# Performance work log

Hardware: AMD Instinct MI355X
Metric: run time of the kernel (lower is better)

Reference implementation:

```python
import jax, jax.numpy as jnp
import numpy as np

K = 20
EPS = 1e-5
NEG_SLOPE = 0.2


def knn_idx(feat, k):
    # feat: (B, N, C). Pairwise neg squared distance, top-k nearest (self included).
    inner = jnp.einsum('bnc,bmc->bnm', feat, feat)          # (B,N,N)
    sq = jnp.sum(feat * feat, axis=-1)                      # (B,N)
    pd = 2.0 * inner - sq[:, :, None] - sq[:, None, :]      # -||xi-xj||^2
    return jax.lax.top_k(pd, k)[1]                          # (B,N,k)


def edge_conv(feat, W, g, b, m, v, k):
    # feat: (B,N,C); W: (O, 2C); BN params over O channels (eval-mode BN).
    idx = knn_idx(feat, k)                                  # (B,N,k)
    nbr = jnp.take_along_axis(feat[:, None, :, :], idx[..., None], axis=2)  # (B,N,k,C)
    ctr = jnp.broadcast_to(feat[:, :, None, :], nbr.shape)
    edge = jnp.concatenate([nbr - ctr, ctr], axis=-1)       # (B,N,k,2C)
    h = jnp.einsum('bnkc,oc->bnko', edge, W)                # 1x1 conv
    h = (h - m) * (g / jnp.sqrt(v + EPS)) + b               # BatchNorm2d (eval)
    h = jnp.where(h >= 0, h, NEG_SLOPE * h)                 # LeakyReLU(0.2)
    return jnp.max(h, axis=2)                               # max over k -> (B,N,O)


def setup_inputs() -> dict:
    key = jax.random.key(0)
    ks = jax.random.split(key, 21)
    B, N, C = 4, 4096, 3
    d = {'x': jax.random.normal(ks[0], (B, N, C), dtype=jnp.float32)}
    dims = [(64, 2 * 3), (64, 2 * 64), (128, 2 * 64), (256, 2 * 128)]
    for i, (o, c) in enumerate(dims, start=1):
        j = 1 + (i - 1) * 5
        d[f'W{i}'] = jax.random.normal(ks[j], (o, c), dtype=jnp.float32) * (1.0 / np.sqrt(c))
        d[f'g{i}'] = jax.random.uniform(ks[j + 1], (o,), minval=0.5, maxval=1.5, dtype=jnp.float32)
        d[f'b{i}'] = jax.random.normal(ks[j + 2], (o,), dtype=jnp.float32) * 0.1
        d[f'm{i}'] = jax.random.normal(ks[j + 3], (o,), dtype=jnp.float32) * 0.1
        d[f'v{i}'] = jax.random.uniform(ks[j + 4], (o,), minval=0.5, maxval=1.5, dtype=jnp.float32)
    return d


def reference(x, W1, g1, b1, m1, v1, W2, g2, b2, m2, v2,
              W3, g3, b3, m3, v3, W4, g4, b4, m4, v4):
    x1 = edge_conv(x, W1, g1, b1, m1, v1, K)    # (B,N,64)
    x2 = edge_conv(x1, W2, g2, b2, m2, v2, K)   # (B,N,64)
    x3 = edge_conv(x2, W3, g3, b3, m3, v3, K)   # (B,N,128)
    x4 = edge_conv(x3, W4, g4, b4, m4, v4, K)   # (B,N,256)
    return x4
```

## Files before the change

### kernel.cpp

```cpp
#include <hip/hip_runtime.h>

#define NTOT 4096
#define NBATCH 4
#define KNN 20
#define JSPLIT 8
#define KMRG 24
#define CSLOTM 512

constexpr float NEG_INF = -3.0e38f;

typedef __attribute__((ext_vector_type(8))) short bf16x8;
typedef __attribute__((ext_vector_type(4))) float f32x4;

__device__ __forceinline__ unsigned pk(float f, int j) {
  unsigned u = __float_as_uint(f);
  u = (u & 0x80000000u) ? ~u : (u | 0x80000000u);
  return (u & 0xFFFFF000u) | (unsigned)j;
}

__device__ __forceinline__ void pins8(unsigned u, unsigned (&tv)[8]) {
  if (u > tv[0]) {
    tv[0] = u;
#pragma unroll
    for (int x = 1; x < 8; x++) {
      unsigned mn = min(tv[0], tv[x]);
      unsigned mx = max(tv[0], tv[x]);
      tv[0] = mn;
      tv[x] = mx;
    }
  }
}

__device__ __forceinline__ void sbf16(float x, ushort& h16, ushort& l16) {
  unsigned u = __float_as_uint(x);
  unsigned h = (u + 0x7FFFu + ((u >> 16) & 1u)) >> 16;
  float hf = __uint_as_float(h << 16);
  float r = x - hf;
  unsigned v = __float_as_uint(r);
  unsigned l = (v + 0x7FFFu + ((v >> 16) & 1u)) >> 16;
  h16 = (ushort)h;
  l16 = (ushort)l;
}

__device__ __forceinline__ void gll16(const void* g, void* l) {
  __builtin_amdgcn_global_load_lds(
      (const __attribute__((address_space(1))) unsigned int*)g,
      (__attribute__((address_space(3))) unsigned int*)l, 16, 0, 0);
}

__global__ void prep_w(const float* __restrict__ W, const float* __restrict__ gg,
                       const float* __restrict__ bb, const float* __restrict__ mm,
                       const float* __restrict__ vv, float* __restrict__ Wc,
                       float* __restrict__ bias, int O, int C) {
  int t = blockIdx.x * 256 + threadIdx.x;
  if (t >= 2 * O * C) return;
  int o2 = t / C, c = t - o2 * C;
  int o = (o2 < O) ? o2 : o2 - O;
  float s = gg[o] * rsqrtf(vv[o] + 1e-5f);
  float w = (o2 < O) ? W[o * 2 * C + c] * s
                     : (W[o * 2 * C + C + c] - W[o * 2 * C + c]) * s;
  Wc[o2 * C + c] = w;
  if (o2 >= O && c == 0) bias[o] = bb[o] - mm[o] * s;
}

__global__ void cvt3_k(const float* __restrict__ f, ushort* __restrict__ hi,
                       ushort* __restrict__ lo) {
  int p = blockIdx.x * 256 + threadIdx.x;
  int pt = p >> 5, dim = p & 31;
  float x = (dim < 3) ? f[pt * 3 + dim] : 0.f;
  ushort h16, l16;
  sbf16(x, h16, l16);
  hi[p] = h16;
  lo[p] = l16;
}

__global__ void sqh3_k(const float* __restrict__ f, float* __restrict__ sqh) {
  int p = blockIdx.x * 256 + threadIdx.x;
  float a = f[(size_t)p * 3 + 0];
  float b2 = f[(size_t)p * 3 + 1];
  float c = f[(size_t)p * 3 + 2];
  sqh[p] = 0.5f * (a * a + b2 * b2 + c * c);
}

template <int C>
__global__ __launch_bounds__(1024, 8) void knn_m(const ushort* __restrict__ Xhi,
                                                 const ushort* __restrict__ Xlo,
                                                 const float* __restrict__ sqh,
                                                 unsigned* __restrict__ cval) {
  constexpr int NK = C / 32;
  constexpr int NJT = NTOT / (128 * JSPLIT);
  constexpr int NSQ = 2 * NJT;
  __shared__ __align__(16) char smem[69632];
  float* sqB = (float*)(smem + 65536);

  int tid = threadIdx.x;
  int raw = blockIdx.x;
  int b = raw & 3;
  int jsp = (raw >> 3) & 3;
  int it = (((raw >> 5) & 15) << 1) | ((raw >> 2) & 1);
  int i0 = it * 128;
  int jpbase = jsp * 1024;
  const ushort* xh = Xhi + (size_t)b * NTOT * C;
  const ushort* xl = Xlo + (size_t)b * NTOT * C;

  int l = tid & 63, wid = tid >> 6;
  int wi = wid & 7, wj = wid >> 3;
  int n = l & 15, quad = l >> 4;
  int xr16 = (n & 7) << 4;

  int t0 = l & 1, t1 = (l >> 1) & 1, t2 = (l >> 2) & 1, t3 = (l >> 3) & 1,
      t4 = (l >> 4) & 1, t5 = (l >> 5) & 1;
  int Rl = (t2 ^ t4) | (t3 << 1) | (t4 << 2) | (t5 << 3);
  int ql = (t0 ^ t2 ^ t4) | ((t1 ^ t3) << 1);

  if (tid < 256) {
    float4 s4 = *(const float4*)&sqh[b * NTOT + jpbase + tid * 4];
    *(float4*)&sqB[tid * 4] = s4;
  }
  __syncthreads();

  unsigned tv[8];
#pragma unroll
  for (int x = 0; x < 8; x++) tv[x] = 0u;

  auto issue = [&](int sn, int kcn, char* buf) {
    int band = wid & 7;
    int R = Rl + band * 16;
    char* ld = buf + band * 1024;
    if (wid < 8) {
      size_t gA = (size_t)(i0 + R) * C + kcn + ql * 8;
      gll16(xh + gA, ld);
      gll16(xl + gA, ld + 8192);
    } else {
      int j0n = jpbase + sn * 128;
      size_t gB = (size_t)(j0n + R) * C + kcn + ql * 8;
      gll16(xh + gB, ld + 16384);
      gll16(xl + gB, ld + 24576);
    }
  };

  issue(0, 0, smem);

  int g = 0;
  for (int s = 0; s < NSQ; s++) {
    int j0 = jpbase + s * 128;

    f32x4 acc[4];
#pragma unroll
    for (int tj = 0; tj < 4; tj++) acc[tj] = (f32x4)(0.f);

    for (int kc = 0; kc < NK; kc++) {
      __builtin_amdgcn_s_barrier();
      int nsn = (kc + 1 < NK) ? s : ((s + 1 == NSQ) ? 0 : s + 1);
      int nkc = (kc + 1 < NK) ? (kc + 1) * 32 : 0;
      issue(nsn, nkc, smem + ((g + 1) & 1) * 32768);
      asm volatile("s_waitcnt vmcnt(2)" ::: "memory");
      __builtin_amdgcn_s_barrier();
      const char* bc = smem + (g & 1) * 32768;

      int arow = wi * 16 + n;
      int aoff = (arow * 64 + quad * 16) ^ xr16;
      bf16x8 ah = *(const bf16x8*)(bc + aoff);
      bf16x8 al_ = *(const bf16x8*)(bc + 8192 + aoff);
#pragma unroll
      for (int tj = 0; tj < 4; tj++) {
        int brow = wj * 64 + tj * 16 + n;
        int boff = (brow * 64 + quad * 16) ^ xr16;
        bf16x8 bh = *(const bf16x8*)(bc + 16384 + boff);
        bf16x8 bl = *(const bf16x8*)(bc + 24576 + boff);
        acc[tj] = __builtin_amdgcn_mfma_f32_16x16x32_bf16(bh, ah, acc[tj], 0, 0, 0);
        acc[tj] = __builtin_amdgcn_mfma_f32_16x16x32_bf16(bh, al_, acc[tj], 0, 0, 0);
        acc[tj] = __builtin_amdgcn_mfma_f32_16x16x32_bf16(bl, ah, acc[tj], 0, 0, 0);
      }
      g++;
    }

    float4 sq4[4];
#pragma unroll
    for (int tj = 0; tj < 4; tj++)
      sq4[tj] = *(const float4*)&sqB[s * 128 + wj * 64 + tj * 16 + quad * 4];
#pragma unroll
    for (int tj = 0; tj < 4; tj++) {
      float v0 = acc[tj][0] - sq4[tj].x;
      float v1 = acc[tj][1] - sq4[tj].y;
      float v2 = acc[tj][2] - sq4[tj].z;
      float v3 = acc[tj][3] - sq4[tj].w;
      float m4 = fmaxf(fmaxf(v0, v1), fmaxf(v2, v3));
      if (pk(m4, 0xFFF) > tv[0]) {
        int jb = j0 + wj * 64 + tj * 16 + quad * 4;
        pins8(pk(v0, jb + 0), tv);
        pins8(pk(v1, jb + 1), tv);
        pins8(pk(v2, jb + 2), tv);
        pins8(pk(v3, jb + 3), tv);
      }
    }

    if (s == NJT - 1 || s == NSQ - 1) {
      int js = jsp * 2 + ((s == NSQ - 1) ? 1 : 0);
      int p = b * NTOT + i0 + wi * 16 + n;
      unsigned* dst = cval + (size_t)p * CSLOTM + js * 64 + wj * 32 + quad * 8;
      uint4 o0, o1;
      o0.x = tv[0]; o0.y = tv[1]; o0.z = tv[2]; o0.w = tv[3];
      o1.x = tv[4]; o1.y = tv[5]; o1.z = tv[6]; o1.w = tv[7];
      *(uint4*)&dst[0] = o0;
      *(uint4*)&dst[4] = o1;
#pragma unroll
      for (int x = 0; x < 8; x++) tv[x] = 0u;
    }
  }
}

template <int C, int NC>
__global__ __launch_bounds__(256) void kref_w(const float* __restrict__ feat,
                                              const unsigned* __restrict__ cval,
                                              int* __restrict__ outidx) {
  int tid = threadIdx.x;
  int lane = tid & 63;
  int pbase = blockIdx.x * 8 + (tid >> 6) * 2;

  unsigned c[2][8];
  int bq[2], iq[2];
#pragma unroll
  for (int pt = 0; pt < 2; pt++) {
    int p = pbase + pt;
    bq[pt] = p >> 12;
    iq[pt] = p & (NTOT - 1);
    uint4 aa = *(const uint4*)&cval[(size_t)p * NC + lane * 8];
    uint4 bb2 = *(const uint4*)&cval[(size_t)p * NC + lane * 8 + 4];
    c[pt][0] = aa.x; c[pt][1] = aa.y; c[pt][2] = aa.z; c[pt][3] = aa.w;
    c[pt][4] = bb2.x; c[pt][5] = bb2.y; c[pt][6] = bb2.z; c[pt][7] = bb2.w;
  }

#define CE(a, bq2)                          \
  {                                         \
    unsigned mx = max(c[pt][a], c[pt][bq2]); \
    unsigned mn = min(c[pt][a], c[pt][bq2]); \
    c[pt][a] = mx;                          \
    c[pt][bq2] = mn;                        \
  }
#pragma unroll
  for (int pt = 0; pt < 2; pt++) {
    CE(0, 1) CE(2, 3) CE(4, 5) CE(6, 7)
    CE(0, 2) CE(1, 3) CE(4, 6) CE(5, 7)
    CE(1, 2) CE(5, 6) CE(0, 4) CE(3, 7)
    CE(1, 5) CE(2, 6)
    CE(1, 4) CE(3, 6)
    CE(2, 4) CE(3, 5)
    CE(3, 4)
  }
#undef CE

  int myj[2] = {-1, -1};
#pragma unroll
  for (int t = 0; t < KMRG; t++) {
#pragma unroll
    for (int pt = 0; pt < 2; pt++) {
      unsigned m = c[pt][0];
#pragma unroll
      for (int s = 1; s < 64; s <<= 1)
        m = max(m, (unsigned)__shfl_xor((int)m, s));
      if (lane == t) myj[pt] = (int)(m & 0xFFFu);
      bool mine = (c[pt][0] == m);
      c[pt][0] = mine ? c[pt][1] : c[pt][0];
      c[pt][1] = mine ? c[pt][2] : c[pt][1];
      c[pt][2] = mine ? c[pt][3] : c[pt][2];
      c[pt][3] = mine ? c[pt][4] : c[pt][3];
      c[pt][4] = mine ? c[pt][5] : c[pt][4];
      c[pt][5] = mine ? c[pt][6] : c[pt][5];
      c[pt][6] = mine ? c[pt][7] : c[pt][6];
      c[pt][7] = mine ? 0u : c[pt][7];
    }
  }

  float myval[2] = {NEG_INF, NEG_INF};
  if constexpr (C == 3) {
#pragma unroll
    for (int pt = 0; pt < 2; pt++) {
      const float* fb = feat + (size_t)bq[pt] * NTOT * 3;
      if (lane < KMRG) {
        float x0 = fb[(size_t)iq[pt] * 3 + 0];
        float x1 = fb[(size_t)iq[pt] * 3 + 1];
        float x2 = fb[(size_t)iq[pt] * 3 + 2];
        float y0 = fb[(size_t)myj[pt] * 3 + 0];
        float y1 = fb[(size_t)myj[pt] * 3 + 1];
        float y2 = fb[(size_t)myj[pt] * 3 + 2];
        float d0 = x0 - y0, d1 = x1 - y1, d2 = x2 - y2;
        myval[pt] = -(d0 * d0 + d1 * d1 + d2 * d2);
      }
    }
  } else {
    constexpr int SL = C / 8;
    int m8 = lane & 7;
    float4 xs[2][SL / 4];
#pragma unroll
    for (int pt = 0; pt < 2; pt++)
#pragma unroll
      for (int q4 = 0; q4 < SL / 4; q4++)
        xs[pt][q4] = *(const float4*)&feat[((size_t)bq[pt] * NTOT + iq[pt]) * C +
                                           m8 * SL + q4 * 4];
#pragma unroll
    for (int ps = 0; ps < KMRG / 8; ps++) {
      int src = ps * 8 + (lane >> 3);
#pragma unroll
      for (int pt = 0; pt < 2; pt++) {
        int j = __shfl(myj[pt], src);
        float d = 0.f;
#pragma unroll
        for (int q4 = 0; q4 < SL / 4; q4++) {
          float4 yv = *(const float4*)&feat[((size_t)bq[pt] * NTOT + j) * C +
                                            m8 * SL + q4 * 4];
          float dx = xs[pt][q4].x - yv.x;
          float dy = xs[pt][q4].y - yv.y;
          float dz = xs[pt][q4].z - yv.z;
          float dw = xs[pt][q4].w - yv.w;
          d += dx * dx + dy * dy + dz * dz + dw * dw;
        }
#pragma unroll
        for (int s = 1; s < 8; s <<= 1) d += __shfl_xor(d, s);
        float sd = __shfl(d, (lane & 7) << 3);
        bool upd = ((lane >> 3) == ps);
        myval[pt] = upd ? -sd : myval[pt];
      }
    }
  }

#pragma unroll
  for (int k = 2; k <= 64; k <<= 1) {
#pragma unroll
    for (int j2 = k >> 1; j2 > 0; j2 >>= 1) {
#pragma unroll
      for (int pt = 0; pt < 2; pt++) {
        float ov = __shfl_xor(myval[pt], j2);
        int oj = __shfl_xor(myj[pt], j2);
        bool ogt = (ov > myval[pt]) || (ov == myval[pt] && oj < myj[pt]);
        bool lower = ((lane & j2) == 0);
        bool desc = ((lane & k) == 0);
        bool take = (desc == (lower == ogt));
        myval[pt] = take ? ov : myval[pt];
        myj[pt] = take ? oj : myj[pt];
      }
    }
  }

#pragma unroll
  for (int pt = 0; pt < 2; pt++)
    if (lane < KNN) outidx[(size_t)(pbase + pt) * KNN + lane] = myj[pt];
}

__global__ __launch_bounds__(256) void gemm128(const float* __restrict__ A,
                                               const float* __restrict__ Wc,
                                               const float* __restrict__ bias,
                                               float* __restrict__ Y, int K, int N2,
                                               int O) {
  constexpr int P = 140;
  __shared__ float As[16 * P];
  __shared__ float Bs[16 * P];
  int tid = threadIdx.x;
  int n0 = blockIdx.x * 128;
  int m0 = blockIdx.y * 128;
  int tx = tid & 15, ty = tid >> 4;
  int aoff = (ty * 8) + (((ty * 8) >> 5) << 2);
  int boff = (tx * 8) + (((tx * 8) >> 5) << 2);
  float acc[8][8];
#pragma unroll
  for (int ii = 0; ii < 8; ii++)
#pragma unroll
    for (int jj = 0; jj < 8; jj++) acc[ii][jj] = 0.f;

  for (int kc = 0; kc < K; kc += 16) {
    __syncthreads();
#pragma unroll
    for (int l = 0; l < 2; l++) {
      int e = tid + 256 * l;
      int rr = e >> 2, c4 = e & 3;
      int sc = rr + ((rr >> 5) << 2);
      float4 va = *(const float4*)&A[(size_t)(m0 + rr) * K + kc + c4 * 4];
      As[(c4 * 4 + 0) * P + sc] = va.x;
      As[(c4 * 4 + 1) * P + sc] = va.y;
      As[(c4 * 4 + 2) * P + sc] = va.z;
      As[(c4 * 4 + 3) * P + sc] = va.w;
      float4 vb = *(const float4*)&Wc[(size_t)(n0 + rr) * K + kc + c4 * 4];
      Bs[(c4 * 4 + 0) * P + sc] = vb.x;
      Bs[(c4 * 4 + 1) * P + sc] = vb.y;
      Bs[(c4 * 4 + 2) * P + sc] = vb.z;
      Bs[(c4 * 4 + 3) * P + sc] = vb.w;
    }
    __syncthreads();
#pragma unroll 8
    for (int k = 0; k < 16; k++) {
      float4 a0 = *(const float4*)&As[k * P + aoff];
      float4 a1 = *(const float4*)&As[k * P + aoff + 4];
      float4 b0 = *(const float4*)&Bs[k * P + boff];
      float4 b1 = *(const float4*)&Bs[k * P + boff + 4];
      float av[8] = {a0.x, a0.y, a0.z, a0.w, a1.x, a1.y, a1.z, a1.w};
      float bv[8] = {b0.x, b0.y, b0.z, b0.w, b1.x, b1.y, b1.z, b1.w};
#pragma unroll
      for (int ii = 0; ii < 8; ii++)
#pragma unroll
        for (int jj = 0; jj < 8; jj++)
          acc[ii][jj] = fmaf(av[ii], bv[jj], acc[ii][jj]);
    }
  }

  int col0 = n0 + tx * 8;
  float bv[8];
#pragma unroll
  for (int jj = 0; jj < 8; jj++) {
    int col = col0 + jj;
    bv[jj] = (col >= O) ? bias[col - O] : 0.f;
  }
#pragma unroll
  for (int ii = 0; ii < 8; ii++) {
    int row = m0 + ty * 8 + ii;
    float4 o0, o1;
    o0.x = acc[ii][0] + bv[0];
    o0.y = acc[ii][1] + bv[1];
    o0.z = acc[ii][2] + bv[2];
    o0.w = acc[ii][3] + bv[3];
    o1.x = acc[ii][4] + bv[4];
    o1.y = acc[ii][5] + bv[5];
    o1.z = acc[ii][6] + bv[6];
    o1.w = acc[ii][7] + bv[7];
    *(float4*)&Y[(size_t)row * N2 + col0] = o0;
    *(float4*)&Y[(size_t)row * N2 + col0 + 4] = o1;
  }
}

__global__ __launch_bounds__(256) void gemm_k(const float* __restrict__ A,
                                              const float* __restrict__ Wc,
                                              const float* __restrict__ bias,
                                              float* __restrict__ Y, int K, int N2,
                                              int O) {
  __shared__ float As[8 * 68];
  __shared__ float Bs[8 * 68];
  int tid = threadIdx.x;
  int n0 = blockIdx.x * 64;
  int m0 = blockIdx.y * 64;
  int tx = tid & 15, ty = tid >> 4;
  float acc[4][4] = {};
  for (int k0 = 0; k0 < K; k0 += 8) {
    __syncthreads();
    {
      int e = tid, mm = e >> 3, kk = e & 7;
      As[kk * 68 + mm] = (k0 + kk < K) ? A[(size_t)(m0 + mm) * K + k0 + kk] : 0.f;
      int nn = mm;
      Bs[kk * 68 + nn] = (k0 + kk < K) ? Wc[(size_t)(n0 + nn) * K + k0 + kk] : 0.f;
      e = tid + 256;
      mm = e >> 3;
      kk = e & 7;
      As[kk * 68 + mm] = (k0 + kk < K) ? A[(size_t)(m0 + mm) * K + k0 + kk] : 0.f;
      nn = mm;
      Bs[kk * 68 + nn] = (k0 + kk < K) ? Wc[(size_t)(n0 + nn) * K + k0 + kk] : 0.f;
    }
    __syncthreads();
#pragma unroll
    for (int kk = 0; kk < 8; kk++) {
      float4 av = *(float4*)&As[kk * 68 + ty * 4];
      float4 bv = *(float4*)&Bs[kk * 68 + tx * 4];
      float a[4] = {av.x, av.y, av.z, av.w};
      float bb2[4] = {bv.x, bv.y, bv.z, bv.w};
#pragma unroll
      for (int ii = 0; ii < 4; ii++)
#pragma unroll
        for (int jj = 0; jj < 4; jj++) acc[ii][jj] += a[ii] * bb2[jj];
    }
  }
  int col = n0 + tx * 4;
  bool isV = (col >= O);
  float b0 = 0.f, b1 = 0.f, b2 = 0.f, b3 = 0.f;
  if (isV) {
    b0 = bias[col + 0 - O];
    b1 = bias[col + 1 - O];
    b2 = bias[col + 2 - O];
    b3 = bias[col + 3 - O];
  }
#pragma unroll
  for (int ii = 0; ii < 4; ii++) {
    int row = m0 + ty * 4 + ii;
    float4 o4;
    o4.x = acc[ii][0] + b0;
    o4.y = acc[ii][1] + b1;
    o4.z = acc[ii][2] + b2;
    o4.w = acc[ii][3] + b3;
    *(float4*)&Y[(size_t)row * N2 + col] = o4;
  }
}

template <int O, int CN>
__global__ __launch_bounds__(256) void gmax_v(const float* __restrict__ Y,
                                              const int* __restrict__ idx,
                                              float* __restrict__ out,
                                              ushort* __restrict__ nxh,
                                              ushort* __restrict__ nxl,
                                              float* __restrict__ nsq) {
  constexpr int T = O / 4;
  constexpr int G = 256 / T;
  int tid = threadIdx.x;
  int p = blockIdx.x * G + tid / T;
  int o4 = (tid % T) * 4;
  int b = p >> 12;
  constexpr int N2 = 2 * O;
  const int* ip = idx + (size_t)p * KNN;
  float4 m = make_float4(NEG_INF, NEG_INF, NEG_INF, NEG_INF);
#pragma unroll
  for (int k = 0; k < KNN; k++) {
    int j = ip[k];
    float4 v = *(const float4*)&Y[((size_t)(b * NTOT + j)) * N2 + o4];
    m.x = fmaxf(m.x, v.x);
    m.y = fmaxf(m.y, v.y);
    m.z = fmaxf(m.z, v.z);
    m.w = fmaxf(m.w, v.w);
  }
  float4 c = *(const float4*)&Y[(size_t)p * N2 + O + o4];
  float4 o;
  o.x = c.x + m.x;
  o.y = c.y + m.y;
  o.z = c.z + m.z;
  o.w = c.w + m.w;
  o.x = (o.x >= 0.f) ? o.x : 0.2f * o.x;
  o.y = (o.y >= 0.f) ? o.y : 0.2f * o.y;
  o.z = (o.z >= 0.f) ? o.z : 0.2f * o.z;
  o.w = (o.w >= 0.f) ? o.w : 0.2f * o.w;
  *(float4*)&out[(size_t)p * O + o4] = o;

  if constexpr (CN != 0) {
    ushort4 h4, l4;
    sbf16(o.x, h4.x, l4.x);
    sbf16(o.y, h4.y, l4.y);
    sbf16(o.z, h4.z, l4.z);
    sbf16(o.w, h4.w, l4.w);
    *(ushort4*)&nxh[(size_t)p * O + o4] = h4;
    *(ushort4*)&nxl[(size_t)p * O + o4] = l4;
    float ss = o.x * o.x + o.y * o.y + o.z * o.z + o.w * o.w;
#pragma unroll
    for (int s = 1; s < T; s <<= 1) ss += __shfl_xor(ss, s);
    if ((tid & (T - 1)) == 0) nsq[p] = 0.5f * ss;
  }
}

template <int C, int O, int CN>
static void run_layer(const float* fin, void* const* w5, float* fout, float* Wc,
                      float* biasb, int* idx, float* Y, float* sqh,
                      unsigned* cval, ushort* Xhi, ushort* Xlo,
                      ushort* nxh, ushort* nxl, hipStream_t stream) {
  const float* W = (const float*)w5[0];
  const float* g = (const float*)w5[1];
  const float* bb = (const float*)w5[2];
  const float* mm = (const float*)w5[3];
  const float* vv = (const float*)w5[4];
  int N2 = 2 * O;
  prep_w<<<(2 * O * C + 255) / 256, 256, 0, stream>>>(W, g, bb, mm, vv, Wc, biasb, O, C);
  if (C == 3) {
    cvt3_k<<<NBATCH * NTOT * 32 / 256, 256, 0, stream>>>(fin, Xhi, Xlo);
    sqh3_k<<<NBATCH * NTOT / 256, 256, 0, stream>>>(fin, sqh);
    knn_m<32><<<NBATCH * 32 * (JSPLIT / 2), 1024, 0, stream>>>(Xhi, Xlo, sqh, cval);
    kref_w<3, 512><<<NBATCH * NTOT / 8, 256, 0, stream>>>(fin, cval, idx);
    dim3 gg(N2 / 64, NBATCH * NTOT / 64);
    gemm_k<<<gg, 256, 0, stream>>>(fin, Wc, biasb, Y, C, N2, O);
  } else {
    knn_m<C><<<NBATCH * 32 * (JSPLIT / 2), 1024, 0, stream>>>(Xhi, Xlo, sqh, cval);
    kref_w<C, 512><<<NBATCH * NTOT / 8, 256, 0, stream>>>(fin, cval, idx);
    dim3 gg(N2 / 128, NBATCH * NTOT / 128);
    gemm128<<<gg, 256, 0, stream>>>(fin, Wc, biasb, Y, C, N2, O);
  }
  gmax_v<O, CN><<<NBATCH * NTOT / (256 / (O / 4)), 256, 0, stream>>>(
      Y, idx, fout, nxh, nxl, sqh);
}

extern "C" void kernel_launch(void* const* d_in, const int* in_sizes, int n_in,
                              void* d_out, int out_size, void* d_ws, size_t ws_size,
                              hipStream_t stream) {
  const float* x = (const float*)d_in[0];
  char* ws = (char*)d_ws;
  float* Wc = (float*)(ws + 0);
  float* biasb = (float*)(ws + 262144);
  int* idx = (int*)(ws + 263168);
  float* sqh = (float*)(ws + 1573888);
  float* Y = (float*)(ws + 1639424);
  float* x1 = (float*)(ws + 35193856);
  float* x2 = (float*)(ws + 39388160);
  float* x3 = (float*)(ws + 43582464);

  unsigned* cval = (unsigned*)Y;
  ushort* X1h = (ushort*)x1;
  ushort* X1l = X1h + (size_t)NBATCH * NTOT * 32;
  ushort* X2h = (ushort*)x2;
  ushort* X2l = X2h + (size_t)NBATCH * NTOT * 64;
  ushort* X3h = (ushort*)x3;
  ushort* X3l = X3h + (size_t)NBATCH * NTOT * 64;
  float* outf = (float*)d_out;
  ushort* X4h = (ushort*)outf;
  ushort* X4l = X4h + (size_t)NBATCH * NTOT * 128;

  run_layer<3, 64, 64>(x, d_in + 1, x1, Wc, biasb, idx, Y, sqh, cval,
                       X1h, X1l, X2h, X2l, stream);
  run_layer<64, 64, 64>(x1, d_in + 6, x2, Wc, biasb, idx, Y, sqh, cval,
                        X2h, X2l, X3h, X3l, stream);
  run_layer<64, 128, 128>(x2, d_in + 11, x3, Wc, biasb, idx, Y, sqh, cval,
                          X3h, X3l, X4h, X4l, stream);
  run_layer<128, 256, 0>(x3, d_in + 16, outf, Wc, biasb, idx, Y, sqh, cval,
                         X4h, X4l, nullptr, nullptr, stream);
}
```

Before: 668.7 us.

## Halve knn block to 512 threads with 2 row tiles per wave

The kNN distance kernel now runs 8 waves per block instead of 16. Each wave computes two 16-row i-tiles against four j-tiles, so every B-operand LDS read feeds twice as many MFMAs. Each wave now issues both the A and B global-to-LDS loads, and the wait count is raised to match. The cost is more accumulator and top-k registers per thread, plus fewer waves per block to hide latency.

```diff
diff --git a/kernel.cpp b/kernel.cpp
--- a/kernel.cpp
+++ b/kernel.cpp
@@ -83,10 +83,10 @@
 }
 
 template <int C>
-__global__ __launch_bounds__(1024, 8) void knn_m(const ushort* __restrict__ Xhi,
-                                                 const ushort* __restrict__ Xlo,
-                                                 const float* __restrict__ sqh,
-                                                 unsigned* __restrict__ cval) {
+__global__ __launch_bounds__(512, 4) void knn_m(const ushort* __restrict__ Xhi,
+                                                const ushort* __restrict__ Xlo,
+                                                const float* __restrict__ sqh,
+                                                unsigned* __restrict__ cval) {
   constexpr int NK = C / 32;
   constexpr int NJT = NTOT / (128 * JSPLIT);
   constexpr int NSQ = 2 * NJT;
@@ -104,7 +104,7 @@
   const ushort* xl = Xlo + (size_t)b * NTOT * C;
 
   int l = tid & 63, wid = tid >> 6;
-  int wi = wid & 7, wj = wid >> 3;
+  int wi = wid & 3, wj = wid >> 2;
   int n = l & 15, quad = l >> 4;
   int xr16 = (n & 7) << 4;
 
@@ -119,24 +119,22 @@
   }
   __syncthreads();
 
-  unsigned tv[8];
-#pragma unroll
-  for (int x = 0; x < 8; x++) tv[x] = 0u;
+  unsigned tv[2][8];
+#pragma unroll
+  for (int ti = 0; ti < 2; ti++)
+#pragma unroll
+    for (int x = 0; x < 8; x++) tv[ti][x] = 0u;
 
   auto issue = [&](int sn, int kcn, char* buf) {
-    int band = wid & 7;
-    int R = Rl + band * 16;
-    char* ld = buf + band * 1024;
-    if (wid < 8) {
-      size_t gA = (size_t)(i0 + R) * C + kcn + ql * 8;
-      gll16(xh + gA, ld);
-      gll16(xl + gA, ld + 8192);
-    } else {
-      int j0n = jpbase + sn * 128;
-      size_t gB = (size_t)(j0n + R) * C + kcn + ql * 8;
-      gll16(xh + gB, ld + 16384);
-      gll16(xl + gB, ld + 24576);
-    }
+    int j0n = jpbase + sn * 128;
+    int R = Rl + wid * 16;
+    size_t gA = (size_t)(i0 + R) * C + kcn + ql * 8;
+    size_t gB = (size_t)(j0n + R) * C + kcn + ql * 8;
+    char* ld = buf + wid * 1024;
+    gll16(xh + gA, ld);
+    gll16(xl + gA, ld + 8192);
+    gll16(xh + gB, ld + 16384);
+    gll16(xl + gB, ld + 24576);
   };
 
   issue(0, 0, smem);
@@ -145,32 +143,41 @@
   for (int s = 0; s < NSQ; s++) {
     int j0 = jpbase + s * 128;
 
-    f32x4 acc[4];
-#pragma unroll
-    for (int tj = 0; tj < 4; tj++) acc[tj] = (f32x4)(0.f);
+    f32x4 acc[4][2];
+#pragma unroll
+    for (int tj = 0; tj < 4; tj++)
+#pragma unroll
+      for (int ti = 0; ti < 2; ti++) acc[tj][ti] = (f32x4)(0.f);
 
     for (int kc = 0; kc < NK; kc++) {
       __builtin_amdgcn_s_barrier();
       int nsn = (kc + 1 < NK) ? s : ((s + 1 == NSQ) ? 0 : s + 1);
       int nkc = (kc + 1 < NK) ? (kc + 1) * 32 : 0;
       issue(nsn, nkc, smem + ((g + 1) & 1) * 32768);
-      asm volatile("s_waitcnt vmcnt(2)" ::: "memory");
+      asm volatile("s_waitcnt vmcnt(4)" ::: "memory");
       __builtin_amdgcn_s_barrier();
       const char* bc = smem + (g & 1) * 32768;
 
-      int arow = wi * 16 + n;
-      int aoff = (arow * 64 + quad * 16) ^ xr16;
-      bf16x8 ah = *(const bf16x8*)(bc + aoff);
-      bf16x8 al_ = *(const bf16x8*)(bc + 8192 + aoff);
+      bf16x8 ah[2], al_[2];
+#pragma unroll
+      for (int ti = 0; ti < 2; ti++) {
+        int row = wi * 32 + ti * 16 + n;
+        int off = (row * 64 + quad * 16) ^ xr16;
+        ah[ti] = *(const bf16x8*)(bc + off);
+        al_[ti] = *(const bf16x8*)(bc + 8192 + off);
+      }
 #pragma unroll
       for (int tj = 0; tj < 4; tj++) {
-        int brow = wj * 64 + tj * 16 + n;
-        int boff = (brow * 64 + quad * 16) ^ xr16;
-        bf16x8 bh = *(const bf16x8*)(bc + 16384 + boff);
-        bf16x8 bl = *(const bf16x8*)(bc + 24576 + boff);
-        acc[tj] = __builtin_amdgcn_mfma_f32_16x16x32_bf16(bh, ah, acc[tj], 0, 0, 0);
-        acc[tj] = __builtin_amdgcn_mfma_f32_16x16x32_bf16(bh, al_, acc[tj], 0, 0, 0);
-        acc[tj] = __builtin_amdgcn_mfma_f32_16x16x32_bf16(bl, ah, acc[tj], 0, 0, 0);
+        int row = wj * 64 + tj * 16 + n;
+        int off = (row * 64 + quad * 16) ^ xr16;
+        bf16x8 bh = *(const bf16x8*)(bc + 16384 + off);
+        bf16x8 bl = *(const bf16x8*)(bc + 24576 + off);
+#pragma unroll
+        for (int ti = 0; ti < 2; ti++) {
+          acc[tj][ti] = __builtin_amdgcn_mfma_f32_16x16x32_bf16(bh, ah[ti], acc[tj][ti], 0, 0, 0);
+          acc[tj][ti] = __builtin_amdgcn_mfma_f32_16x16x32_bf16(bh, al_[ti], acc[tj][ti], 0, 0, 0);
+          acc[tj][ti] = __builtin_amdgcn_mfma_f32_16x16x32_bf16(bl, ah[ti], acc[tj][ti], 0, 0, 0);
+        }
       }
       g++;
     }
@@ -180,32 +187,38 @@
     for (int tj = 0; tj < 4; tj++)
       sq4[tj] = *(const float4*)&sqB[s * 128 + wj * 64 + tj * 16 + quad * 4];
 #pragma unroll
-    for (int tj = 0; tj < 4; tj++) {
-      float v0 = acc[tj][0] - sq4[tj].x;
-      float v1 = acc[tj][1] - sq4[tj].y;
-      float v2 = acc[tj][2] - sq4[tj].z;
-      float v3 = acc[tj][3] - sq4[tj].w;
-      float m4 = fmaxf(fmaxf(v0, v1), fmaxf(v2, v3));
-      if (pk(m4, 0xFFF) > tv[0]) {
-        int jb = j0 + wj * 64 + tj * 16 + quad * 4;
-        pins8(pk(v0, jb + 0), tv);
-        pins8(pk(v1, jb + 1), tv);
-        pins8(pk(v2, jb + 2), tv);
-        pins8(pk(v3, jb + 3), tv);
+    for (int ti = 0; ti < 2; ti++) {
+#pragma unroll
+      for (int tj = 0; tj < 4; tj++) {
+        float v0 = acc[tj][ti][0] - sq4[tj].x;
+        float v1 = acc[tj][ti][1] - sq4[tj].y;
+        float v2 = acc[tj][ti][2] - sq4[tj].z;
+        float v3 = acc[tj][ti][3] - sq4[tj].w;
+        float m4 = fmaxf(fmaxf(v0, v1), fmaxf(v2, v3));
+        if (pk(m4, 0xFFF) > tv[ti][0]) {
+          int jb = j0 + wj * 64 + tj * 16 + quad * 4;
+          pins8(pk(v0, jb + 0), tv[ti]);
+          pins8(pk(v1, jb + 1), tv[ti]);
+          pins8(pk(v2, jb + 2), tv[ti]);
+          pins8(pk(v3, jb + 3), tv[ti]);
+        }
       }
     }
 
     if (s == NJT - 1 || s == NSQ - 1) {
       int js = jsp * 2 + ((s == NSQ - 1) ? 1 : 0);
-      int p = b * NTOT + i0 + wi * 16 + n;
-      unsigned* dst = cval + (size_t)p * CSLOTM + js * 64 + wj * 32 + quad * 8;
-      uint4 o0, o1;
-      o0.x = tv[0]; o0.y = tv[1]; o0.z = tv[2]; o0.w = tv[3];
-      o1.x = tv[4]; o1.y = tv[5]; o1.z = tv[6]; o1.w = tv[7];
-      *(uint4*)&dst[0] = o0;
-      *(uint4*)&dst[4] = o1;
-#pragma unroll
-      for (int x = 0; x < 8; x++) tv[x] = 0u;
+#pragma unroll
+      for (int ti = 0; ti < 2; ti++) {
+        int p = b * NTOT + i0 + wi * 32 + ti * 16 + n;
+        unsigned* dst = cval + (size_t)p * CSLOTM + js * 64 + wj * 32 + quad * 8;
+        uint4 o0, o1;
+        o0.x = tv[ti][0]; o0.y = tv[ti][1]; o0.z = tv[ti][2]; o0.w = tv[ti][3];
+        o1.x = tv[ti][4]; o1.y = tv[ti][5]; o1.z = tv[ti][6]; o1.w = tv[ti][7];
+        *(uint4*)&dst[0] = o0;
+        *(uint4*)&dst[4] = o1;
+#pragma unroll
+        for (int x = 0; x < 8; x++) tv[ti][x] = 0u;
+      }
     }
   }
 }
@@ -553,12 +566,12 @@
   if (C == 3) {
     cvt3_k<<<NBATCH * NTOT * 32 / 256, 256, 0, stream>>>(fin, Xhi, Xlo);
     sqh3_k<<<NBATCH * NTOT / 256, 256, 0, stream>>>(fin, sqh);
-    knn_m<32><<<NBATCH * 32 * (JSPLIT / 2), 1024, 0, stream>>>(Xhi, Xlo, sqh, cval);
+    knn_m<32><<<NBATCH * 32 * (JSPLIT / 2), 512, 0, stream>>>(Xhi, Xlo, sqh, cval);
     kref_w<3, 512><<<NBATCH * NTOT / 8, 256, 0, stream>>>(fin, cval, idx);
     dim3 gg(N2 / 64, NBATCH * NTOT / 64);
     gemm_k<<<gg, 256, 0, stream>>>(fin, Wc, biasb, Y, C, N2, O);
   } else {
-    knn_m<C><<<NBATCH * 32 * (JSPLIT / 2), 1024, 0, stream>>>(Xhi, Xlo, sqh, cval);
+    knn_m<C><<<NBATCH * 32 * (JSPLIT / 2), 512, 0, stream>>>(Xhi, Xlo, sqh, cval);
     kref_w<C, 512><<<NBATCH * NTOT / 8, 256, 0, stream>>>(fin, cval, idx);
     dim3 gg(N2 / 128, NBATCH * NTOT / 128);
     gemm128<<<gg, 256, 0, stream>>>(fin, Wc, biasb, Y, C, N2, O);
```

After: 650.2 us. -2.8%, faster.
